# Kernel tuning notes

Measured on AMD Instinct MI355X. Metric: run time of the kernel, lower is better.

Reference implementation:

```python
import jax, jax.numpy as jnp
import numpy as np

B, S, H, A = 32, 4096, 512, 256

def setup_inputs() -> dict:
    key = jax.random.key(0)
    ks = jax.random.split(key, 8)
    sH = 1.0 / np.sqrt(H)
    sA = 1.0 / np.sqrt(A)
    return {
        "encoder_outputs": jax.random.normal(ks[0], (B, S, H), dtype=jnp.float32),
        "decoder_hidden": jax.random.normal(ks[1], (B, H), dtype=jnp.float32),
        "W_enc": jax.random.uniform(ks[2], (H, A), jnp.float32, -sH, sH),
        "b_enc": jax.random.uniform(ks[3], (A,), jnp.float32, -sH, sH),
        "W_dec": jax.random.uniform(ks[4], (H, A), jnp.float32, -sH, sH),
        "b_dec": jax.random.uniform(ks[5], (A,), jnp.float32, -sH, sH),
        "W_e": jax.random.uniform(ks[6], (A,), jnp.float32, -sA, sA),
        "b_e": jax.random.uniform(ks[7], (), jnp.float32, -sA, sA),
    }

def reference(encoder_outputs, decoder_hidden, W_enc, b_enc, W_dec, b_dec, W_e, b_e):
    # [B,S,A] encoder projection
    enc_p = jnp.einsum('bsh,ha->bsa', encoder_outputs, W_enc) + b_enc
    # [B,1,A] decoder projection broadcast over S
    dec_p = (decoder_hidden @ W_dec + b_dec)[:, None, :]
    scores = jnp.einsum('bsa,a->bs', jnp.tanh(enc_p + dec_p), W_e) + b_e  # [B,S]
    attn = jax.nn.softmax(scores, axis=1)                                 # [B,S]
    context = jnp.einsum('bs,bsh->bh', attn, encoder_outputs)             # [B,H]
    return context, attn
```

## Files before the change

kernel.cpp:

```cpp
#include <hip/hip_runtime.h>
#include <hip/hip_bf16.h>
#include <stdint.h>


typedef __attribute__((ext_vector_type(4))) float f32x4;
typedef __attribute__((ext_vector_type(8))) short short8;

#define B_  32
#define S_  4096
#define H_  512
#define A_  256
#define CHUNKS_ 64

#define WS_WT     0
#define WS_BIAS   262144
#define WS_SCORES 294912
#define WS_M      819200
#define WS_L      827392
#define WS_PART   835584

#define STRIDE_ 520

static __device__ __forceinline__ short f2bf(float f) {
  union { float f; uint32_t u; } v; v.f = f;
  uint32_t r = (v.u + 0x7FFFu + ((v.u >> 16) & 1u)) >> 16;
  return (short)(uint16_t)r;
}
static __device__ __forceinline__ float bf2f(uint32_t lo16) {
  union { uint32_t u; float f; } v; v.u = lo16 << 16; return v.f;
}

__global__ __launch_bounds__(256) void prep_kernel(
    const float* __restrict__ dh, const float* __restrict__ W_enc,
    const float* __restrict__ b_enc, const float* __restrict__ W_dec,
    const float* __restrict__ b_dec, unsigned short* __restrict__ WT,
    float* __restrict__ bias) {
  __shared__ float dh_s[512];
  __shared__ unsigned short tile[64 * 66];
  const int tid = threadIdx.x;
  if (blockIdx.x < 32) {
    const int b = blockIdx.x;
    dh_s[tid]       = dh[(size_t)b * H_ + tid];
    dh_s[tid + 256] = dh[(size_t)b * H_ + tid + 256];
    __syncthreads();
    float s[4] = {0.f, 0.f, 0.f, 0.f};
    for (int k = 0; k < H_; k += 32) {
      #pragma unroll
      for (int j = 0; j < 32; ++j)
        s[j & 3] = fmaf(dh_s[k + j], W_dec[(size_t)(k + j) * A_ + tid], s[j & 3]);
    }
    bias[b * A_ + tid] = s[0] + s[1] + s[2] + s[3] + b_enc[tid] + b_dec[tid];
  } else {
    const int t = blockIdx.x - 32;
    const int kt = t >> 2, nt2 = t & 3;
    #pragma unroll
    for (int i = 0; i < 16; ++i) {
      int idx = tid + i * 256;
      int kk = idx >> 6, nn = idx & 63;
      tile[kk * 66 + nn] =
          (unsigned short)f2bf(W_enc[(size_t)(kt * 64 + kk) * A_ + nt2 * 64 + nn]);
    }
    __syncthreads();
    #pragma unroll
    for (int i = 0; i < 16; ++i) {
      int idx = tid + i * 256;
      int nn = idx >> 6, kk = idx & 63;
      WT[(size_t)(nt2 * 64 + nn) * H_ + kt * 64 + kk] = tile[kk * 66 + nn];
    }
  }
}

__global__ __launch_bounds__(256, 2) void fused_kernel(
    const float* __restrict__ enc, const unsigned short* __restrict__ WT,
    const float* __restrict__ bias, const float* __restrict__ We,
    float* __restrict__ scores, float* __restrict__ wsm,
    float* __restrict__ wsl, float* __restrict__ part) {
  __shared__ __align__(16) unsigned short stash[64 * STRIDE_];
  __shared__ float s_ps[4][64];
  __shared__ float s_e[64];

  const int tid = threadIdx.x, w = tid >> 6, lane = tid & 63;
  const int lm = lane & 15, lq = lane >> 4;
  const int b = blockIdx.x >> 6;
  const int chunk = blockIdx.x & 63;
  const int srow0 = blockIdx.x * 64;

  f32x4 acc[4][4];
  #pragma unroll
  for (int mt = 0; mt < 4; ++mt)
    #pragma unroll
    for (int nt = 0; nt < 4; ++nt)
      acc[mt][nt] = (f32x4){0.f, 0.f, 0.f, 0.f};

  const int arow = tid >> 2, akoff = (tid & 3) * 8;
  const float* aptr = enc + (size_t)(srow0 + arow) * H_ + akoff;
  unsigned short* swp = &stash[arow * STRIDE_ + akoff];

  const unsigned short* bptr = WT + (size_t)((w * 4) * 16 + lm) * H_ + lq * 8;

  short8 Bring[3][4];
  float4 abuf0_a, abuf0_b, abuf1_a, abuf1_b;

  abuf0_a = *(const float4*)aptr;
  abuf0_b = *(const float4*)(aptr + 4);
  {
    short8 sv;
    sv[0] = f2bf(abuf0_a.x); sv[1] = f2bf(abuf0_a.y); sv[2] = f2bf(abuf0_a.z); sv[3] = f2bf(abuf0_a.w);
    sv[4] = f2bf(abuf0_b.x); sv[5] = f2bf(abuf0_b.y); sv[6] = f2bf(abuf0_b.z); sv[7] = f2bf(abuf0_b.w);
    *(short8*)swp = sv;
  }
  abuf1_a = *(const float4*)(aptr + 32);
  abuf1_b = *(const float4*)(aptr + 36);
  #pragma unroll
  for (int j = 0; j < 4; ++j) {
    Bring[0][j] = *(const short8*)(bptr + (size_t)j * 16 * H_);
    Bring[1][j] = *(const short8*)(bptr + (size_t)j * 16 * H_ + 32);
  }
  __syncthreads();

  #pragma unroll
  for (int k = 0; k < 16; ++k) {
    const int kel = k * 32;
    float4 na_a, na_b;
    if (k + 2 < 16) {
      na_a = *(const float4*)(aptr + (k + 2) * 32);
      na_b = *(const float4*)(aptr + (k + 2) * 32 + 4);
    }
    if (k + 2 < 16) {
      #pragma unroll
      for (int j = 0; j < 4; ++j)
        Bring[(k + 2) % 3][j] = *(const short8*)(bptr + (size_t)j * 16 * H_ + (k + 2) * 32);
    }
    #pragma unroll
    for (int mt = 0; mt < 4; ++mt) {
      short8 af = *(const short8*)&stash[(mt * 16 + lm) * STRIDE_ + kel + lq * 8];
      #pragma unroll
      for (int j = 0; j < 4; ++j)
        acc[mt][j] = __builtin_amdgcn_mfma_f32_16x16x32_bf16(af, Bring[k % 3][j], acc[mt][j], 0, 0, 0);
    }
    if (k < 15) {
      float4 ca = (k & 1) ? abuf0_a : abuf1_a;
      float4 cb = (k & 1) ? abuf0_b : abuf1_b;
      short8 sv;
      sv[0] = f2bf(ca.x); sv[1] = f2bf(ca.y); sv[2] = f2bf(ca.z); sv[3] = f2bf(ca.w);
      sv[4] = f2bf(cb.x); sv[5] = f2bf(cb.y); sv[6] = f2bf(cb.z); sv[7] = f2bf(cb.w);
      *(short8*)(swp + (k + 1) * 32) = sv;
    }
    if (k + 2 < 16) {
      if (k & 1) { abuf1_a = na_a; abuf1_b = na_b; }
      else       { abuf0_a = na_a; abuf0_b = na_b; }
    }
    __syncthreads();
  }

  float psum[4][4] = {{0,0,0,0},{0,0,0,0},{0,0,0,0},{0,0,0,0}};
  #pragma unroll
  for (int j = 0; j < 4; ++j) {
    const int col = (w * 4 + j) * 16 + lm;
    const float dp = bias[b * A_ + col];
    const float wv = We[col];
    #pragma unroll
    for (int mt = 0; mt < 4; ++mt)
      #pragma unroll
      for (int r = 0; r < 4; ++r) {
        float x = acc[mt][j][r] + dp;
        float e = __expf(2.0f * x);
        float t = 1.0f - 2.0f * __builtin_amdgcn_rcpf(e + 1.0f);
        psum[mt][r] = fmaf(t, wv, psum[mt][r]);
      }
  }
  #pragma unroll
  for (int o = 1; o < 16; o <<= 1)
    #pragma unroll
    for (int mt = 0; mt < 4; ++mt)
      #pragma unroll
      for (int r = 0; r < 4; ++r)
        psum[mt][r] += __shfl_xor(psum[mt][r], o, 64);
  if (lm == 0) {
    #pragma unroll
    for (int mt = 0; mt < 4; ++mt)
      #pragma unroll
      for (int r = 0; r < 4; ++r)
        s_ps[w][mt * 16 + lq * 4 + r] = psum[mt][r];
  }
  __syncthreads();

  if (tid < 64) {
    const float sc = s_ps[0][tid] + s_ps[1][tid] + s_ps[2][tid] + s_ps[3][tid];
    scores[srow0 + tid] = sc;
    float m = sc;
    #pragma unroll
    for (int o = 1; o < 64; o <<= 1) m = fmaxf(m, __shfl_xor(m, o, 64));
    const float e = __expf(sc - m);
    float l = e;
    #pragma unroll
    for (int o = 1; o < 64; o <<= 1) l += __shfl_xor(l, o, 64);
    s_e[tid] = e;
    if (tid == 0) {
      wsm[b * CHUNKS_ + chunk] = m;
      wsl[b * CHUNKS_ + chunk] = l;
    }
  }
  __syncthreads();

  float cx0 = 0.f, cx1 = 0.f;
  #pragma unroll 8
  for (int row = 0; row < 64; ++row) {
    uint32_t pv = *(const uint32_t*)&stash[row * STRIDE_ + (tid << 1)];
    float wr = s_e[row];
    cx0 = fmaf(wr, bf2f(pv & 0xffffu), cx0);
    cx1 = fmaf(wr, bf2f(pv >> 16), cx1);
  }
  float2 o2; o2.x = cx0; o2.y = cx1;
  *(float2*)&part[(size_t)(b * CHUNKS_ + chunk) * H_ + (tid << 1)] = o2;
}

__global__ __launch_bounds__(256) void finalize_kernel(
    const float* __restrict__ scores, const float* __restrict__ wsm,
    const float* __restrict__ wsl, const float* __restrict__ part,
    float* __restrict__ ctx, float* __restrict__ attn) {
  __shared__ float wgt[CHUNKS_];
  __shared__ float s_ml[2];
  const int b = blockIdx.x, tid = threadIdx.x;
  if (tid < 64) {
    float mc = wsm[b * CHUNKS_ + tid];
    float lc = wsl[b * CHUNKS_ + tid];
    float M = mc;
    #pragma unroll
    for (int o = 1; o < 64; o <<= 1) M = fmaxf(M, __shfl_xor(M, o, 64));
    float wv = __expf(mc - M);
    float Lp = wv * lc;
    #pragma unroll
    for (int o = 1; o < 64; o <<= 1) Lp += __shfl_xor(Lp, o, 64);
    wgt[tid] = wv;
    if (tid == 0) { s_ml[0] = M; s_ml[1] = Lp; }
  }
  __syncthreads();
  const float M = s_ml[0];
  const float invL = 1.0f / s_ml[1];

  #pragma unroll
  for (int hh = 0; hh < 2; ++hh) {
    const int h = tid + hh * 256;
    float s = 0.f;
    #pragma unroll 8
    for (int c = 0; c < CHUNKS_; ++c)
      s = fmaf(wgt[c], part[(size_t)(b * CHUNKS_ + c) * H_ + h], s);
    ctx[(size_t)b * H_ + h] = s * invL;
  }
  #pragma unroll
  for (int i = 0; i < 16; ++i) {
    const int s_ = tid + i * 256;
    attn[(size_t)b * S_ + s_] = __expf(scores[(size_t)b * S_ + s_] - M) * invL;
  }
}

extern "C" void kernel_launch(void* const* d_in, const int* in_sizes, int n_in,
                              void* d_out, int out_size, void* d_ws, size_t ws_size,
                              hipStream_t stream) {
  const float* enc   = (const float*)d_in[0];
  const float* dh    = (const float*)d_in[1];
  const float* W_enc = (const float*)d_in[2];
  const float* b_enc = (const float*)d_in[3];
  const float* W_dec = (const float*)d_in[4];
  const float* b_dec = (const float*)d_in[5];
  const float* W_e   = (const float*)d_in[6];

  char* ws = (char*)d_ws;
  unsigned short* WT = (unsigned short*)(ws + WS_WT);
  float* bias   = (float*)(ws + WS_BIAS);
  float* scores = (float*)(ws + WS_SCORES);
  float* wsm    = (float*)(ws + WS_M);
  float* wsl    = (float*)(ws + WS_L);
  float* part   = (float*)(ws + WS_PART);

  float* ctx  = (float*)d_out;
  float* attn = (float*)d_out + B_ * H_;

  prep_kernel<<<dim3(64), dim3(256), 0, stream>>>(dh, W_enc, b_enc, W_dec, b_dec, WT, bias);
  fused_kernel<<<dim3(2048), dim3(256), 0, stream>>>(enc, WT, bias, W_e, scores, wsm, wsl, part);
  finalize_kernel<<<dim3(32), dim3(256), 0, stream>>>(scores, wsm, wsl, part, ctx, attn);
}
```

Measured before the change: 419.7 us.

## Deepen A prefetch ring, use lighter LDS barriers, and parallelize finalize

In the fused kernel, the two-slot A-register double buffer becomes a three-slot ring, so global loads are issued three k-steps ahead. __syncthreads is replaced by a custom barrier that waits only on LDS counters, which lets outstanding global prefetches stay in flight across the barrier, and the last-iteration barrier is dropped. The fused kernel now stores exp(score - chunk max) instead of raw scores, so finalize only rescales by the chunk weight. Finalize is split across 256 blocks (8 per batch), each handling a 64-column slice of the context reduction over four chunk groups and a 512-element slice of attn, to improve parallelism in that small tail kernel.

```diff
diff --git a/kernel.cpp b/kernel.cpp
--- a/kernel.cpp
+++ b/kernel.cpp
@@ -28,6 +28,12 @@
 }
 static __device__ __forceinline__ float bf2f(uint32_t lo16) {
   union { uint32_t u; float f; } v; v.u = lo16 << 16; return v.f;
+}
+
+static __device__ __forceinline__ void lds_barrier() {
+  asm volatile("s_waitcnt lgkmcnt(0)" ::: "memory");
+  __builtin_amdgcn_s_barrier();
+  asm volatile("" ::: "memory");
 }
 
 __global__ __launch_bounds__(256) void prep_kernel(
@@ -99,32 +105,32 @@
   const unsigned short* bptr = WT + (size_t)((w * 4) * 16 + lm) * H_ + lq * 8;
 
   short8 Bring[3][4];
-  float4 abuf0_a, abuf0_b, abuf1_a, abuf1_b;
-
-  abuf0_a = *(const float4*)aptr;
-  abuf0_b = *(const float4*)(aptr + 4);
-  {
-    short8 sv;
-    sv[0] = f2bf(abuf0_a.x); sv[1] = f2bf(abuf0_a.y); sv[2] = f2bf(abuf0_a.z); sv[3] = f2bf(abuf0_a.w);
-    sv[4] = f2bf(abuf0_b.x); sv[5] = f2bf(abuf0_b.y); sv[6] = f2bf(abuf0_b.z); sv[7] = f2bf(abuf0_b.w);
-    *(short8*)swp = sv;
-  }
-  abuf1_a = *(const float4*)(aptr + 32);
-  abuf1_b = *(const float4*)(aptr + 36);
+  float4 Aring[3][2];
+
+  float4 a0a = *(const float4*)aptr;
+  float4 a0b = *(const float4*)(aptr + 4);
+  Aring[1][0] = *(const float4*)(aptr + 1 * 32);
+  Aring[1][1] = *(const float4*)(aptr + 1 * 32 + 4);
+  Aring[2][0] = *(const float4*)(aptr + 2 * 32);
+  Aring[2][1] = *(const float4*)(aptr + 2 * 32 + 4);
   #pragma unroll
   for (int j = 0; j < 4; ++j) {
     Bring[0][j] = *(const short8*)(bptr + (size_t)j * 16 * H_);
     Bring[1][j] = *(const short8*)(bptr + (size_t)j * 16 * H_ + 32);
   }
-  __syncthreads();
+  {
+    short8 sv;
+    sv[0] = f2bf(a0a.x); sv[1] = f2bf(a0a.y); sv[2] = f2bf(a0a.z); sv[3] = f2bf(a0a.w);
+    sv[4] = f2bf(a0b.x); sv[5] = f2bf(a0b.y); sv[6] = f2bf(a0b.z); sv[7] = f2bf(a0b.w);
+    *(short8*)swp = sv;
+  }
+  lds_barrier();
 
   #pragma unroll
   for (int k = 0; k < 16; ++k) {
-    const int kel = k * 32;
-    float4 na_a, na_b;
-    if (k + 2 < 16) {
-      na_a = *(const float4*)(aptr + (k + 2) * 32);
-      na_b = *(const float4*)(aptr + (k + 2) * 32 + 4);
+    if (k + 3 < 16) {
+      Aring[(k + 3) % 3][0] = *(const float4*)(aptr + (k + 3) * 32);
+      Aring[(k + 3) % 3][1] = *(const float4*)(aptr + (k + 3) * 32 + 4);
     }
     if (k + 2 < 16) {
       #pragma unroll
@@ -133,24 +139,20 @@
     }
     #pragma unroll
     for (int mt = 0; mt < 4; ++mt) {
-      short8 af = *(const short8*)&stash[(mt * 16 + lm) * STRIDE_ + kel + lq * 8];
+      short8 af = *(const short8*)&stash[(mt * 16 + lm) * STRIDE_ + k * 32 + lq * 8];
       #pragma unroll
       for (int j = 0; j < 4; ++j)
         acc[mt][j] = __builtin_amdgcn_mfma_f32_16x16x32_bf16(af, Bring[k % 3][j], acc[mt][j], 0, 0, 0);
     }
     if (k < 15) {
-      float4 ca = (k & 1) ? abuf0_a : abuf1_a;
-      float4 cb = (k & 1) ? abuf0_b : abuf1_b;
+      float4 ca = Aring[(k + 1) % 3][0];
+      float4 cb = Aring[(k + 1) % 3][1];
       short8 sv;
       sv[0] = f2bf(ca.x); sv[1] = f2bf(ca.y); sv[2] = f2bf(ca.z); sv[3] = f2bf(ca.w);
       sv[4] = f2bf(cb.x); sv[5] = f2bf(cb.y); sv[6] = f2bf(cb.z); sv[7] = f2bf(cb.w);
       *(short8*)(swp + (k + 1) * 32) = sv;
-    }
-    if (k + 2 < 16) {
-      if (k & 1) { abuf1_a = na_a; abuf1_b = na_b; }
-      else       { abuf0_a = na_a; abuf0_b = na_b; }
-    }
-    __syncthreads();
+      lds_barrier();
+    }
   }
 
   float psum[4][4] = {{0,0,0,0},{0,0,0,0},{0,0,0,0},{0,0,0,0}};
@@ -183,11 +185,10 @@
       for (int r = 0; r < 4; ++r)
         s_ps[w][mt * 16 + lq * 4 + r] = psum[mt][r];
   }
-  __syncthreads();
+  lds_barrier();
 
   if (tid < 64) {
     const float sc = s_ps[0][tid] + s_ps[1][tid] + s_ps[2][tid] + s_ps[3][tid];
-    scores[srow0 + tid] = sc;
     float m = sc;
     #pragma unroll
     for (int o = 1; o < 64; o <<= 1) m = fmaxf(m, __shfl_xor(m, o, 64));
@@ -196,12 +197,13 @@
     #pragma unroll
     for (int o = 1; o < 64; o <<= 1) l += __shfl_xor(l, o, 64);
     s_e[tid] = e;
+    scores[srow0 + tid] = e;
     if (tid == 0) {
       wsm[b * CHUNKS_ + chunk] = m;
       wsl[b * CHUNKS_ + chunk] = l;
     }
   }
-  __syncthreads();
+  lds_barrier();
 
   float cx0 = 0.f, cx1 = 0.f;
   #pragma unroll 8
@@ -216,12 +218,14 @@
 }
 
 __global__ __launch_bounds__(256) void finalize_kernel(
-    const float* __restrict__ scores, const float* __restrict__ wsm,
+    const float* __restrict__ scores_e, const float* __restrict__ wsm,
     const float* __restrict__ wsl, const float* __restrict__ part,
     float* __restrict__ ctx, float* __restrict__ attn) {
   __shared__ float wgt[CHUNKS_];
-  __shared__ float s_ml[2];
-  const int b = blockIdx.x, tid = threadIdx.x;
+  __shared__ float s_inv;
+  __shared__ float csum[4][64];
+  const int b = blockIdx.x >> 3, j = blockIdx.x & 7;
+  const int tid = threadIdx.x;
   if (tid < 64) {
     float mc = wsm[b * CHUNKS_ + tid];
     float lc = wsl[b * CHUNKS_ + tid];
@@ -233,25 +237,29 @@
     #pragma unroll
     for (int o = 1; o < 64; o <<= 1) Lp += __shfl_xor(Lp, o, 64);
     wgt[tid] = wv;
-    if (tid == 0) { s_ml[0] = M; s_ml[1] = Lp; }
+    if (tid == 0) s_inv = 1.0f / Lp;
   }
   __syncthreads();
-  const float M = s_ml[0];
-  const float invL = 1.0f / s_ml[1];
-
-  #pragma unroll
-  for (int hh = 0; hh < 2; ++hh) {
-    const int h = tid + hh * 256;
+  const float invL = s_inv;
+
+  {
+    const int h = j * 64 + (tid & 63), g = tid >> 6;
     float s = 0.f;
-    #pragma unroll 8
-    for (int c = 0; c < CHUNKS_; ++c)
+    #pragma unroll 4
+    for (int c = g * 16; c < g * 16 + 16; ++c)
       s = fmaf(wgt[c], part[(size_t)(b * CHUNKS_ + c) * H_ + h], s);
-    ctx[(size_t)b * H_ + h] = s * invL;
-  }
-  #pragma unroll
-  for (int i = 0; i < 16; ++i) {
-    const int s_ = tid + i * 256;
-    attn[(size_t)b * S_ + s_] = __expf(scores[(size_t)b * S_ + s_] - M) * invL;
+    csum[g][tid & 63] = s;
+  }
+  __syncthreads();
+  if (tid < 64) {
+    float s = csum[0][tid] + csum[1][tid] + csum[2][tid] + csum[3][tid];
+    ctx[(size_t)b * H_ + j * 64 + tid] = s * invL;
+  }
+
+  #pragma unroll
+  for (int i = 0; i < 2; ++i) {
+    const int s_ = j * 512 + tid + i * 256;
+    attn[(size_t)b * S_ + s_] = scores_e[(size_t)b * S_ + s_] * wgt[s_ >> 6] * invL;
   }
 }
 
@@ -279,5 +287,5 @@
 
   prep_kernel<<<dim3(64), dim3(256), 0, stream>>>(dh, W_enc, b_enc, W_dec, b_dec, WT, bias);
   fused_kernel<<<dim3(2048), dim3(256), 0, stream>>>(enc, WT, bias, W_e, scores, wsm, wsl, part);
-  finalize_kernel<<<dim3(32), dim3(256), 0, stream>>>(scores, wsm, wsl, part, ctx, attn);
-}
+  finalize_kernel<<<dim3(256), dim3(256), 0, stream>>>(scores, wsm, wsl, part, ctx, attn);
+}
```

Measured after the change: 414.2 us. No clear change (-1.3%).
